# Kernel tuning notes

Hardware: AMD Instinct MI355X
Metric: run time of the kernel (lower is better)

Reference implementation:

```python
import jax, jax.numpy as jnp
import numpy as np

N_NODES = 50000
N_EDGES = 800000
IN_FEATS = 128
H_FEATS = 128
NUM_CLASSES = 64


def _linear_params(key, fan_in, fan_out):
    kw, kb = jax.random.split(key)
    bound = 1.0 / np.sqrt(fan_in)
    W = jax.random.uniform(kw, (fan_out, fan_in), minval=-bound, maxval=bound, dtype=jnp.float32)
    b = jax.random.uniform(kb, (fan_out,), minval=-bound, maxval=bound, dtype=jnp.float32)
    return W, b


def setup_inputs() -> dict:
    key = jax.random.key(0)
    k_feat, k_src, k_dst, k1, k2, k3 = jax.random.split(key, 6)
    in_feat = jax.random.normal(k_feat, (N_NODES, IN_FEATS), dtype=jnp.float32)
    src = jax.random.randint(k_src, (N_EDGES,), 0, N_NODES, dtype=jnp.int32)
    dst = jax.random.randint(k_dst, (N_EDGES,), 0, N_NODES, dtype=jnp.int32)
    W1, b1 = _linear_params(k1, IN_FEATS, H_FEATS)
    W2, b2 = _linear_params(k2, H_FEATS, H_FEATS)
    W3, b3 = _linear_params(k3, H_FEATS, NUM_CLASSES)
    return {"in_feat": in_feat, "W1": W1, "b1": b1, "W2": W2, "b2": b2,
            "W3": W3, "b3": b3, "src": src, "dst": dst}


def reference(in_feat, W1, b1, W2, b2, W3, b3, src, dst):
    N = in_feat.shape[0]

    def gin_layer(x, W, b):
        # DGL GINConv with eps=0: (x + sum of in-neighbor messages) -> Linear
        agg = jax.ops.segment_sum(x[src], dst, num_segments=N)  # [N, d]
        return jax.nn.relu((x + agg) @ W.T + b)

    h = gin_layer(in_feat, W1, b1)
    h = gin_layer(h, W2, b2)
    h = gin_layer(h, W3, b3)
    return h
```

## Files before the change

### kernel.cpp

```cpp
#include <hip/hip_runtime.h>

typedef _Float16 half8 __attribute__((ext_vector_type(8)));
typedef float floatx4 __attribute__((ext_vector_type(4)));

union AB { uint4 u; half8 h; };
union H2 { unsigned int u; _Float16 h[2]; };
union US16 { uint4 u[2]; unsigned short s[16]; };

#define CAPLOG 6
#define CAP 64

__global__ __launch_bounds__(256) void histA_k(const int* __restrict__ dst,
                                               int* __restrict__ histG, int E, int nbins) {
    __shared__ int h[256];
    int t = threadIdx.x;
    h[t] = 0;
    __syncthreads();
    int per = (E + 255) / 256;
    int beg = blockIdx.x * per;
    int end = min(E, beg + per);
    for (int e = beg + t; e < end; e += 256)
        atomicAdd(&h[dst[e] >> 8], 1);
    __syncthreads();
    for (int i = t; i < nbins; i += 256)
        histG[i * 256 + blockIdx.x] = h[i];
}

__global__ __launch_bounds__(1024) void scan1_k(const int* __restrict__ x,
                                                int* __restrict__ inc,
                                                int* __restrict__ partial, int n) {
    __shared__ int sd[1024];
    int t = threadIdx.x;
    int v = blockIdx.x * 1024 + t;
    sd[t] = (v < n) ? x[v] : 0;
    __syncthreads();
    for (int off = 1; off < 1024; off <<= 1) {
        int val = (t >= off) ? sd[t - off] : 0;
        __syncthreads();
        sd[t] += val;
        __syncthreads();
    }
    if (v < n) inc[v] = sd[t];
    if (t == 1023) partial[blockIdx.x] = sd[1023];
}

__global__ void scan2_k(int* __restrict__ partial, int nb) {
    int lane = threadIdx.x;
    int v = (lane < nb) ? partial[lane] : 0;
    for (int off = 1; off < 64; off <<= 1) {
        int n = __shfl_up(v, off, 64);
        if (lane >= off) v += n;
    }
    int ex = __shfl_up(v, 1, 64);
    if (lane == 0) ex = 0;
    if (lane < nb) partial[lane] = ex;
}

__global__ void scan3_excl_k(const int* __restrict__ inc, const int* __restrict__ partial,
                             const int* __restrict__ orig, int* __restrict__ excl, int n) {
    int v = blockIdx.x * blockDim.x + threadIdx.x;
    if (v < n) excl[v] = inc[v] + partial[v >> 10] - orig[v];
}

__global__ __launch_bounds__(256) void scatterA_k(const int* __restrict__ src,
                                                  const int* __restrict__ dst,
                                                  const int* __restrict__ excl,
                                                  unsigned int* __restrict__ binned,
                                                  int E, int nbins) {
    __shared__ int cur[256];
    int t = threadIdx.x;
    for (int i = t; i < nbins; i += 256) cur[i] = excl[i * 256 + blockIdx.x];
    __syncthreads();
    int per = (E + 255) / 256;
    int beg = blockIdx.x * per;
    int end = min(E, beg + per);
    for (int e = beg + t; e < end; e += 256) {
        int d = dst[e];
        int s = src[e];
        int pos = atomicAdd(&cur[d >> 8], 1);
        binned[pos] = ((unsigned int)(d & 255) << 16) | (unsigned int)s;
    }
}

__global__ __launch_bounds__(256) void binB_k(const unsigned int* __restrict__ binned,
                                              const int* __restrict__ excl,
                                              unsigned short* __restrict__ col,
                                              int* __restrict__ cnt,
                                              int N, int E, int nbins) {
    __shared__ unsigned short lcol[256 * CAP];
    __shared__ int lcnt[256];
    int t = threadIdx.x;
    int b = blockIdx.x;
    unsigned int* lcol32 = (unsigned int*)lcol;
    for (int i = t; i < 256 * CAP / 2; i += 256) lcol32[i] = 0xFFFFFFFFu;
    lcnt[t] = 0;
    __syncthreads();
    int beg = excl[b * 256];
    int end = (b == nbins - 1) ? E : excl[(b + 1) * 256];
    for (int e = beg + t; e < end; e += 256) {
        unsigned int u = binned[e];
        int dl = u >> 16;
        int pos = atomicAdd(&lcnt[dl], 1);
        if (pos < CAP) lcol[(dl << CAPLOG) + pos] = (unsigned short)(u & 0xFFFFu);
    }
    __syncthreads();
    int base = b << 8;
    int nodes = min(256, N - base);
    uint4* colg = (uint4*)(col + ((size_t)base << CAPLOG));
    const uint4* coll = (const uint4*)lcol;
    for (int i = t; i < nodes * 8; i += 256) colg[i] = coll[i];
    for (int i = t; i < nodes; i += 256) cnt[base + i] = lcnt[i];
}

__global__ void cast_feat_k(const float* __restrict__ X, _Float16* __restrict__ Y, int n4) {
    int i = blockIdx.x * blockDim.x + threadIdx.x;
    if (i < n4) {
        float4 v = reinterpret_cast<const float4*>(X)[i];
        union { uint2 u; _Float16 h[4]; } o;
        o.h[0] = (_Float16)v.x; o.h[1] = (_Float16)v.y;
        o.h[2] = (_Float16)v.z; o.h[3] = (_Float16)v.w;
        reinterpret_cast<uint2*>(Y)[i] = o.u;
    }
}

__global__ void cast_w_k(const float* __restrict__ W1, const float* __restrict__ W2,
                         const float* __restrict__ W3, _Float16* __restrict__ O1,
                         _Float16* __restrict__ O2, _Float16* __restrict__ O3,
                         int n4_1, int n4_2, int n4_3) {
    int i = blockIdx.x * blockDim.x + threadIdx.x;
    const float* W;
    _Float16* O;
    int j;
    if (i < n4_1) { W = W1; O = O1; j = i; }
    else if (i < n4_1 + n4_2) { W = W2; O = O2; j = i - n4_1; }
    else if (i < n4_1 + n4_2 + n4_3) { W = W3; O = O3; j = i - n4_1 - n4_2; }
    else return;
    float4 v = reinterpret_cast<const float4*>(W)[j];
    union { uint2 u; _Float16 h[4]; } o;
    o.h[0] = (_Float16)v.x; o.h[1] = (_Float16)v.y;
    o.h[2] = (_Float16)v.z; o.h[3] = (_Float16)v.w;
    reinterpret_cast<uint2*>(O)[j] = o.u;
}

__global__ void zero_rows_k(unsigned int* __restrict__ a, unsigned int* __restrict__ b, int off) {
    int t = threadIdx.x;
    a[off + t] = 0u;
    b[off + t] = 0u;
}

__global__ __launch_bounds__(256) void aggregate_k(const _Float16* __restrict__ X,
                                                   const int* __restrict__ cnt,
                                                   const unsigned short* __restrict__ col,
                                                   _Float16* __restrict__ Y,
                                                   int nnodes) {
    int w = blockIdx.x * 4 + (threadIdx.x >> 6);
    int lane = threadIdx.x & 63;
    if (w >= nnodes) return;
    const unsigned int* X32 = reinterpret_cast<const unsigned int*>(X);
    int deg = cnt[w];
    if (deg > CAP) deg = CAP;
    int degp = (deg + 15) & ~15;
    const unsigned short* c = col + ((size_t)w << CAPLOG);

    float a[8], b[8];
#pragma unroll
    for (int j = 0; j < 8; j++) { a[j] = 0.f; b[j] = 0.f; }

    for (int e = 0; e < degp; e += 16) {
        US16 ix;
        ix.u[0] = *reinterpret_cast<const uint4*>(c + e);
        ix.u[1] = *reinterpret_cast<const uint4*>(c + e + 8);
        H2 u[16];
#pragma unroll
        for (int j = 0; j < 16; j++) {
            int s = (int)ix.s[j];
            s = (s < nnodes) ? s : nnodes;
            u[j].u = X32[(size_t)s * 64 + lane];
        }
#pragma unroll
        for (int j = 0; j < 8; j++) {
            a[j] += (float)u[j].h[0] + (float)u[j + 8].h[0];
            b[j] += (float)u[j].h[1] + (float)u[j + 8].h[1];
        }
    }

    H2 xs, r;
    xs.u = X32[(size_t)w * 64 + lane];
    float s0 = ((a[0] + a[1]) + (a[2] + a[3])) + ((a[4] + a[5]) + (a[6] + a[7]));
    float s1 = ((b[0] + b[1]) + (b[2] + b[3])) + ((b[4] + b[5]) + (b[6] + b[7]));
    r.h[0] = (_Float16)((float)xs.h[0] + s0);
    r.h[1] = (_Float16)((float)xs.h[1] + s1);
    reinterpret_cast<unsigned int*>(Y)[(size_t)w * 64 + lane] = r.u;
}

template <int NOUT, bool OUT_F32>
__global__ __launch_bounds__(256) void gemm_mfma_k(const _Float16* __restrict__ Y,
                                                   const _Float16* __restrict__ Wh,
                                                   const float* __restrict__ bias,
                                                   void* __restrict__ out, int nnodes) {
    constexpr int NT = NOUT / 16;
    constexpr int WSTR = 136;
    __shared__ _Float16 Wl[NOUT * WSTR];
    __shared__ float Bl[NOUT];

    const int t = threadIdx.x;
    for (int p = t; p < NOUT * 16; p += 256) {
        int f = p >> 4;
        int kq = (p & 15) * 8;
        uint4 u = *reinterpret_cast<const uint4*>(Wh + f * 128 + kq);
        *reinterpret_cast<uint4*>(&Wl[f * WSTR + kq]) = u;
    }
    if (t < NOUT) Bl[t] = bias[t];
    __syncthreads();

    const int wave = t >> 6;
    const int lane = t & 63;
    const int quad = lane >> 4;
    const int fcol = lane & 15;
    const int m_base = (blockIdx.x * 4 + wave) * 16;
    const int row = m_base + fcol;
    const bool rowok = row < nnodes;

    floatx4 acc[NT];
#pragma unroll
    for (int ft = 0; ft < NT; ft++) acc[ft] = (floatx4){0.f, 0.f, 0.f, 0.f};

    const uint4* Yrow = reinterpret_cast<const uint4*>(Y + (size_t)row * 128);
#pragma unroll
    for (int step = 0; step < 4; step++) {
        AB a;
        if (rowok) a.u = Yrow[step * 4 + quad];
        else       a.u = make_uint4(0u, 0u, 0u, 0u);
#pragma unroll
        for (int ft = 0; ft < NT; ft++) {
            half8 b = *reinterpret_cast<const half8*>(
                &Wl[(ft * 16 + fcol) * WSTR + step * 32 + quad * 8]);
            acc[ft] = __builtin_amdgcn_mfma_f32_16x16x32_f16(a.h, b, acc[ft], 0, 0, 0);
        }
    }

#pragma unroll
    for (int ft = 0; ft < NT; ft++) {
        int f = ft * 16 + fcol;
        float bv = Bl[f];
#pragma unroll
        for (int r = 0; r < 4; r++) {
            int node = m_base + quad * 4 + r;
            if (node < nnodes) {
                float v = fmaxf(acc[ft][r] + bv, 0.f);
                if (OUT_F32)
                    reinterpret_cast<float*>(out)[(size_t)node * NOUT + f] = v;
                else
                    reinterpret_cast<_Float16*>(out)[(size_t)node * NOUT + f] = (_Float16)v;
            }
        }
    }
}

extern "C" void kernel_launch(void* const* d_in, const int* in_sizes, int n_in,
                              void* d_out, int out_size, void* d_ws, size_t ws_size,
                              hipStream_t stream) {
    const float* in_feat = (const float*)d_in[0];
    const float* W1 = (const float*)d_in[1];
    const float* b1 = (const float*)d_in[2];
    const float* W2 = (const float*)d_in[3];
    const float* b2 = (const float*)d_in[4];
    const float* W3 = (const float*)d_in[5];
    const float* b3 = (const float*)d_in[6];
    const int* src = (const int*)d_in[7];
    const int* dst = (const int*)d_in[8];
    float* out = (float*)d_out;

    const int N = in_sizes[0] / 128;
    const int E = in_sizes[7];
    const int szW1 = in_sizes[1];
    const int szW2 = in_sizes[3];
    const int szW3 = in_sizes[5];
    const int nbins = (N + 255) >> 8;
    const int nhist = nbins * 256;

    char* p = (char*)d_ws;
    int* cnt = (int*)p;               p += (size_t)N * 4;
    unsigned short* col = (unsigned short*)p; p += (size_t)N * CAP * 2;
    int* histG = (int*)p;             p += (size_t)nhist * 4;
    int* incS = (int*)p;              p += (size_t)nhist * 4;
    int* excl = (int*)p;              p += (size_t)nhist * 4;
    int* partial = (int*)p;           p += 256;
    unsigned int* binned = (unsigned int*)p; p += (size_t)E * 4;
    _Float16* hX = (_Float16*)p;      p += (size_t)(N + 1) * 128 * 2;
    _Float16* hB = (_Float16*)p;      p += (size_t)(N + 1) * 128 * 2;
    _Float16* W1h = (_Float16*)p;     p += (size_t)szW1 * 2;
    _Float16* W2h = (_Float16*)p;     p += (size_t)szW2 * 2;
    _Float16* W3h = (_Float16*)p;     p += (size_t)szW3 * 2;

    const int nblk_scan = (nhist + 1023) / 1024;

    histA_k<<<256, 256, 0, stream>>>(dst, histG, E, nbins);
    scan1_k<<<nblk_scan, 1024, 0, stream>>>(histG, incS, partial, nhist);
    scan2_k<<<1, 64, 0, stream>>>(partial, nblk_scan);
    scan3_excl_k<<<(nhist + 255) / 256, 256, 0, stream>>>(incS, partial, histG, excl, nhist);
    scatterA_k<<<256, 256, 0, stream>>>(src, dst, excl, binned, E, nbins);
    binB_k<<<nbins, 256, 0, stream>>>(binned, excl, col, cnt, N, E, nbins);

    cast_feat_k<<<(N * 128 / 4 + 255) / 256, 256, 0, stream>>>(in_feat, hX, N * 128 / 4);
    {
        int n4 = (szW1 + szW2 + szW3) / 4;
        cast_w_k<<<(n4 + 255) / 256, 256, 0, stream>>>(W1, W2, W3, W1h, W2h, W3h,
                                                       szW1 / 4, szW2 / 4, szW3 / 4);
    }
    zero_rows_k<<<1, 64, 0, stream>>>((unsigned int*)hX, (unsigned int*)hB, N * 64);

    const int nblk_agg = (N + 3) / 4;
    const int nblk_gemm = (N + 63) / 64;
    aggregate_k<<<nblk_agg, 256, 0, stream>>>(hX, cnt, col, hB, N);
    gemm_mfma_k<128, false><<<nblk_gemm, 256, 0, stream>>>(hB, W1h, b1, hX, N);
    aggregate_k<<<nblk_agg, 256, 0, stream>>>(hX, cnt, col, hB, N);
    gemm_mfma_k<128, false><<<nblk_gemm, 256, 0, stream>>>(hB, W2h, b2, hX, N);
    aggregate_k<<<nblk_agg, 256, 0, stream>>>(hX, cnt, col, hB, N);
    gemm_mfma_k<64, true><<<nblk_gemm, 256, 0, stream>>>(hB, W3h, b3, out, N);
}
```

Measured before the change: 262.1 us.

## Split aggregation into feature quarters across blocks and fuse init kernels

```diff
diff --git a/kernel.cpp b/kernel.cpp
--- a/kernel.cpp
+++ b/kernel.cpp
@@ -2,10 +2,11 @@
 
 typedef _Float16 half8 __attribute__((ext_vector_type(8)));
 typedef float floatx4 __attribute__((ext_vector_type(4)));
+typedef unsigned int uintx4 __attribute__((ext_vector_type(4)));
 
 union AB { uint4 u; half8 h; };
 union H2 { unsigned int u; _Float16 h[2]; };
-union US16 { uint4 u[2]; unsigned short s[16]; };
+union US16 { uintx4 u[2]; unsigned short s[16]; };
 
 #define CAPLOG 6
 #define CAP 64
@@ -112,40 +113,31 @@
     for (int i = t; i < nodes; i += 256) cnt[base + i] = lcnt[i];
 }
 
-__global__ void cast_feat_k(const float* __restrict__ X, _Float16* __restrict__ Y, int n4) {
+__global__ void init_k(const float* __restrict__ F, const float* __restrict__ W1,
+                       const float* __restrict__ W2, const float* __restrict__ W3,
+                       _Float16* __restrict__ hX, _Float16* __restrict__ W1h,
+                       _Float16* __restrict__ W2h, _Float16* __restrict__ W3h,
+                       _Float16* __restrict__ hB,
+                       int n4f, int n4w1, int n4w2, int n4w3, int zoff4) {
     int i = blockIdx.x * blockDim.x + threadIdx.x;
-    if (i < n4) {
-        float4 v = reinterpret_cast<const float4*>(X)[i];
-        union { uint2 u; _Float16 h[4]; } o;
-        o.h[0] = (_Float16)v.x; o.h[1] = (_Float16)v.y;
-        o.h[2] = (_Float16)v.z; o.h[3] = (_Float16)v.w;
-        reinterpret_cast<uint2*>(Y)[i] = o.u;
-    }
-}
-
-__global__ void cast_w_k(const float* __restrict__ W1, const float* __restrict__ W2,
-                         const float* __restrict__ W3, _Float16* __restrict__ O1,
-                         _Float16* __restrict__ O2, _Float16* __restrict__ O3,
-                         int n4_1, int n4_2, int n4_3) {
-    int i = blockIdx.x * blockDim.x + threadIdx.x;
-    const float* W;
+    const float* X;
     _Float16* O;
     int j;
-    if (i < n4_1) { W = W1; O = O1; j = i; }
-    else if (i < n4_1 + n4_2) { W = W2; O = O2; j = i - n4_1; }
-    else if (i < n4_1 + n4_2 + n4_3) { W = W3; O = O3; j = i - n4_1 - n4_2; }
-    else return;
-    float4 v = reinterpret_cast<const float4*>(W)[j];
+    if (i < n4f) { X = F; O = hX; j = i; }
+    else if (i < n4f + n4w1) { X = W1; O = W1h; j = i - n4f; }
+    else if (i < n4f + n4w1 + n4w2) { X = W2; O = W2h; j = i - n4f - n4w1; }
+    else if (i < n4f + n4w1 + n4w2 + n4w3) { X = W3; O = W3h; j = i - n4f - n4w1 - n4w2; }
+    else {
+        int z = i - (n4f + n4w1 + n4w2 + n4w3);
+        if (z < 16) ((uint4*)hX)[zoff4 + z] = make_uint4(0, 0, 0, 0);
+        else if (z < 32) ((uint4*)hB)[zoff4 + z - 16] = make_uint4(0, 0, 0, 0);
+        return;
+    }
+    float4 v = reinterpret_cast<const float4*>(X)[j];
     union { uint2 u; _Float16 h[4]; } o;
     o.h[0] = (_Float16)v.x; o.h[1] = (_Float16)v.y;
     o.h[2] = (_Float16)v.z; o.h[3] = (_Float16)v.w;
     reinterpret_cast<uint2*>(O)[j] = o.u;
-}
-
-__global__ void zero_rows_k(unsigned int* __restrict__ a, unsigned int* __restrict__ b, int off) {
-    int t = threadIdx.x;
-    a[off + t] = 0u;
-    b[off + t] = 0u;
 }
 
 __global__ __launch_bounds__(256) void aggregate_k(const _Float16* __restrict__ X,
@@ -153,44 +145,50 @@
                                                    const unsigned short* __restrict__ col,
                                                    _Float16* __restrict__ Y,
                                                    int nnodes) {
-    int w = blockIdx.x * 4 + (threadIdx.x >> 6);
+    int b = blockIdx.x;
+    int q = (b & 7) >> 1;
+    int ng = ((b >> 3) << 1) | (b & 1);
     int lane = threadIdx.x & 63;
-    if (w >= nnodes) return;
-    const unsigned int* X32 = reinterpret_cast<const unsigned int*>(X);
-    int deg = cnt[w];
+    int fl = lane & 15;
+    int node = ng * 16 + (threadIdx.x >> 6) * 4 + (lane >> 4);
+    if (node >= nnodes) return;
+    const unsigned int* X32 = (const unsigned int*)X;
+    int qoff = q << 4;
+
+    int deg = cnt[node];
     if (deg > CAP) deg = CAP;
     int degp = (deg + 15) & ~15;
-    const unsigned short* c = col + ((size_t)w << CAPLOG);
-
-    float a[8], b[8];
-#pragma unroll
-    for (int j = 0; j < 8; j++) { a[j] = 0.f; b[j] = 0.f; }
+    const unsigned short* c = col + ((size_t)node << CAPLOG);
+
+    float a[8], bb[8];
+#pragma unroll
+    for (int j = 0; j < 8; j++) { a[j] = 0.f; bb[j] = 0.f; }
 
     for (int e = 0; e < degp; e += 16) {
         US16 ix;
-        ix.u[0] = *reinterpret_cast<const uint4*>(c + e);
-        ix.u[1] = *reinterpret_cast<const uint4*>(c + e + 8);
+        ix.u[0] = *reinterpret_cast<const uintx4*>(c + e);
+        ix.u[1] = *reinterpret_cast<const uintx4*>(c + e + 8);
         H2 u[16];
 #pragma unroll
         for (int j = 0; j < 16; j++) {
             int s = (int)ix.s[j];
             s = (s < nnodes) ? s : nnodes;
-            u[j].u = X32[(size_t)s * 64 + lane];
+            u[j].u = X32[(size_t)s * 64 + qoff + fl];
         }
 #pragma unroll
         for (int j = 0; j < 8; j++) {
             a[j] += (float)u[j].h[0] + (float)u[j + 8].h[0];
-            b[j] += (float)u[j].h[1] + (float)u[j + 8].h[1];
+            bb[j] += (float)u[j].h[1] + (float)u[j + 8].h[1];
         }
     }
 
     H2 xs, r;
-    xs.u = X32[(size_t)w * 64 + lane];
+    xs.u = X32[(size_t)node * 64 + qoff + fl];
     float s0 = ((a[0] + a[1]) + (a[2] + a[3])) + ((a[4] + a[5]) + (a[6] + a[7]));
-    float s1 = ((b[0] + b[1]) + (b[2] + b[3])) + ((b[4] + b[5]) + (b[6] + b[7]));
+    float s1 = ((bb[0] + bb[1]) + (bb[2] + bb[3])) + ((bb[4] + bb[5]) + (bb[6] + bb[7]));
     r.h[0] = (_Float16)((float)xs.h[0] + s0);
     r.h[1] = (_Float16)((float)xs.h[1] + s1);
-    reinterpret_cast<unsigned int*>(Y)[(size_t)w * 64 + lane] = r.u;
+    __builtin_nontemporal_store(r.u, reinterpret_cast<unsigned int*>(Y) + (size_t)node * 64 + qoff + fl);
 }
 
 template <int NOUT, bool OUT_F32>
@@ -302,15 +300,17 @@
     scatterA_k<<<256, 256, 0, stream>>>(src, dst, excl, binned, E, nbins);
     binB_k<<<nbins, 256, 0, stream>>>(binned, excl, col, cnt, N, E, nbins);
 
-    cast_feat_k<<<(N * 128 / 4 + 255) / 256, 256, 0, stream>>>(in_feat, hX, N * 128 / 4);
     {
-        int n4 = (szW1 + szW2 + szW3) / 4;
-        cast_w_k<<<(n4 + 255) / 256, 256, 0, stream>>>(W1, W2, W3, W1h, W2h, W3h,
-                                                       szW1 / 4, szW2 / 4, szW3 / 4);
-    }
-    zero_rows_k<<<1, 64, 0, stream>>>((unsigned int*)hX, (unsigned int*)hB, N * 64);
-
-    const int nblk_agg = (N + 3) / 4;
+        int n4f = N * 128 / 4;
+        int total = n4f + szW1 / 4 + szW2 / 4 + szW3 / 4 + 32;
+        init_k<<<(total + 255) / 256, 256, 0, stream>>>(in_feat, W1, W2, W3,
+                                                        hX, W1h, W2h, W3h, hB,
+                                                        n4f, szW1 / 4, szW2 / 4, szW3 / 4,
+                                                        N * 16);
+    }
+
+    const int ngrp = (N + 15) / 16;
+    const int nblk_agg = 8 * ((ngrp + 1) / 2);
     const int nblk_gemm = (N + 63) / 64;
     aggregate_k<<<nblk_agg, 256, 0, stream>>>(hX, cnt, col, hB, N);
     gemm_mfma_k<128, false><<<nblk_gemm, 256, 0, stream>>>(hB, W1h, b1, hX, N);
```

Result: no change. 263.9 us (+0.7%).
